# Performance work log

Measured on AMD Instinct MI355X. Metric: run time of the kernel, lower is better.

Reference implementation:

```python
import jax, jax.numpy as jnp
import numpy as np

B, P, E = 16, 1024, 768
HID, HEADS = 768, 12
DH = HID // HEADS  # 64
EPS = 1e-5


def setup_inputs() -> dict:
    key = jax.random.key(0)
    ks = jax.random.split(key, 4)
    return {
        "x": jax.random.normal(ks[0], (B, P, E), dtype=jnp.float32),
        "ln_weight": jnp.ones((P, E), dtype=jnp.float32),
        "ln_bias": jnp.zeros((P, E), dtype=jnp.float32),
        "qkv": jax.random.normal(ks[1], (E, 3 * HID), dtype=jnp.float32),
        "lin_w": jax.random.normal(ks[2], (HID, E), dtype=jnp.float32) * 0.02,
        "lin_b": jax.random.normal(ks[3], (E,), dtype=jnp.float32) * 0.02,
    }


def reference(x, ln_weight, ln_bias, qkv, lin_w, lin_b):
    # LayerNorm over the last TWO dims (patches, emb), per torch nn.LayerNorm((P, E))
    mean = jnp.mean(x, axis=(-2, -1), keepdims=True)
    var = jnp.var(x, axis=(-2, -1), keepdims=True)
    xn = (x - mean) / jnp.sqrt(var + EPS) * ln_weight + ln_bias

    # QKV projection: [B,P,E] @ [E,3*HID] -> [B,P,3*HID]
    proj = xn @ qkv
    # view(B,P,heads,-1) then permute -> [B,heads,P,3*DH]; chunk along last dim
    proj = proj.reshape(B, P, HEADS, 3 * DH).transpose(0, 2, 1, 3)
    q, k, v = proj[..., :DH], proj[..., DH:2 * DH], proj[..., 2 * DH:]

    # Softmax-free attention: (Q K^T) V
    atten = jnp.einsum("bhqd,bhkd->bhqk", q, k)  # [B,H,P,P]
    out = jnp.einsum("bhqk,bhkd->bhqd", atten, v)  # [B,H,P,DH]

    out = out.transpose(0, 2, 1, 3).reshape(B, P, HID)
    # dropout p=0.0 (eval) -> identity
    out = jax.nn.relu(out @ lin_w + lin_b)
    return out + x
```

## Files before the change

kernel.cpp:

```cpp
#include <hip/hip_runtime.h>
#include <hip/hip_bf16.h>
#include <cstdint>

#define BB   16
#define PP   1024
#define EE   768
#define HID  768
#define NH   12
#define DH   64
#define NPB  (PP * EE)
#define MROWS (BB * PP)

typedef __bf16 bf16_t;
typedef __bf16 bf16x8 __attribute__((ext_vector_type(8)));
typedef float  f32x4  __attribute__((ext_vector_type(4)));

__device__ __forceinline__ void gld16(const void* g, void* l) {
    __builtin_amdgcn_global_load_lds(
        (const __attribute__((address_space(1))) void*)(uintptr_t)g,
        (__attribute__((address_space(3))) void*)(uint32_t)(uintptr_t)l,
        16, 0, 0);
}

__global__ __launch_bounds__(256) void stats1_kernel(const float* __restrict__ x,
                                                     float* __restrict__ part) {
    int bid = blockIdx.x;
    int b = bid >> 6, s = bid & 63;
    const float4* xp = (const float4*)(x + (size_t)b * NPB + (size_t)s * 12288);
    float sum = 0.f, ss = 0.f;
#pragma unroll
    for (int i = 0; i < 12; ++i) {
        float4 v = xp[i * 256 + threadIdx.x];
        sum += v.x + v.y + v.z + v.w;
        ss  += v.x * v.x + v.y * v.y + v.z * v.z + v.w * v.w;
    }
#pragma unroll
    for (int off = 32; off > 0; off >>= 1) {
        sum += __shfl_down(sum, off, 64);
        ss  += __shfl_down(ss,  off, 64);
    }
    __shared__ float tmp[8];
    int wave = threadIdx.x >> 6, lane = threadIdx.x & 63;
    if (lane == 0) { tmp[wave * 2] = sum; tmp[wave * 2 + 1] = ss; }
    __syncthreads();
    if (threadIdx.x == 0) {
        part[bid * 2]     = tmp[0] + tmp[2] + tmp[4] + tmp[6];
        part[bid * 2 + 1] = tmp[1] + tmp[3] + tmp[5] + tmp[7];
    }
}

__global__ __launch_bounds__(256) void prep_kernel(const float* __restrict__ qkvw,
                                                   const float* __restrict__ linw,
                                                   const float* __restrict__ part,
                                                   bf16_t* __restrict__ qkvT,
                                                   bf16_t* __restrict__ lwT,
                                                   float* __restrict__ stats) {
    int bid = blockIdx.x;
    if (bid < 6912) {
        int idx = bid * 256 + threadIdx.x;
        int c = idx / 768, r = idx - c * 768;
        qkvT[idx] = (bf16_t)qkvw[(size_t)r * 2304 + c];
    } else if (bid < 9216) {
        int idx = (bid - 6912) * 256 + threadIdx.x;
        int c = idx / 768, r = idx - c * 768;
        lwT[idx] = (bf16_t)linw[(size_t)r * 768 + c];
    } else {
        int wave = threadIdx.x >> 6, lane = threadIdx.x & 63;
#pragma unroll
        for (int j = 0; j < 4; ++j) {
            int b = wave * 4 + j;
            float sum = part[(b * 64 + lane) * 2];
            float ss  = part[(b * 64 + lane) * 2 + 1];
#pragma unroll
            for (int off = 32; off > 0; off >>= 1) {
                sum += __shfl_down(sum, off, 64);
                ss  += __shfl_down(ss,  off, 64);
            }
            if (lane == 0) {
                const float inv_n = 1.f / (float)NPB;
                float mean = sum * inv_n;
                float var  = ss * inv_n - mean * mean;
                stats[b * 2]     = mean;
                stats[b * 2 + 1] = rsqrtf(var + 1e-5f);
            }
        }
    }
}

__global__ __launch_bounds__(256) void ln_apply_kernel(const float* __restrict__ x,
                                                       const float* __restrict__ lnw,
                                                       const float* __restrict__ lnb,
                                                       const float* __restrict__ stats,
                                                       bf16_t* __restrict__ xn) {
    int i = (blockIdx.x * 256 + threadIdx.x) * 8;
    int b = i / NPB;
    int r = i - b * NPB;
    float mean = stats[b * 2], rstd = stats[b * 2 + 1];
    float4 x0 = *(const float4*)(x + i),     x1 = *(const float4*)(x + i + 4);
    float4 w0 = *(const float4*)(lnw + r),   w1 = *(const float4*)(lnw + r + 4);
    float4 c0 = *(const float4*)(lnb + r),   c1 = *(const float4*)(lnb + r + 4);
    union { bf16_t h[8]; uint4 u; } o;
    o.h[0] = (bf16_t)((x0.x - mean) * rstd * w0.x + c0.x);
    o.h[1] = (bf16_t)((x0.y - mean) * rstd * w0.y + c0.y);
    o.h[2] = (bf16_t)((x0.z - mean) * rstd * w0.z + c0.z);
    o.h[3] = (bf16_t)((x0.w - mean) * rstd * w0.w + c0.w);
    o.h[4] = (bf16_t)((x1.x - mean) * rstd * w1.x + c1.x);
    o.h[5] = (bf16_t)((x1.y - mean) * rstd * w1.y + c1.y);
    o.h[6] = (bf16_t)((x1.z - mean) * rstd * w1.z + c1.z);
    o.h[7] = (bf16_t)((x1.w - mean) * rstd * w1.w + c1.w);
    *(uint4*)(xn + i) = o.u;
}

template <int KDIM>
__device__ __forceinline__ void gemm_core_128(const bf16_t* __restrict__ A,
                                              const bf16_t* __restrict__ Bt,
                                              int mBase, int nBase,
                                              f32x4 acc[4][4],
                                              bf16_t* As, bf16_t* Bs) {
    const int t = threadIdx.x;
    const int lane = t & 63, wave = t >> 6;
    const int wm = wave >> 1, wn = wave & 1;
    const int m16 = lane & 15, quad = lane >> 4;

    const int sr = t >> 3, s8 = t & 7;
    const bf16_t* pa[4]; const bf16_t* pb[4];
#pragma unroll
    for (int i = 0; i < 4; ++i) {
        int row = i * 32 + sr;
        int g = (s8 - (row & 7)) & 7;
        pa[i] = A  + (size_t)(mBase + row) * KDIM + g * 8;
        pb[i] = Bt + (size_t)(nBase + row) * KDIM + g * 8;
    }

    int raOff[4][2], rbOff[4][2];
#pragma unroll
    for (int i = 0; i < 4; ++i) {
        int ra = wm * 64 + i * 16 + m16;
        int rb = wn * 64 + i * 16 + m16;
#pragma unroll
        for (int ks = 0; ks < 2; ++ks) {
            raOff[i][ks] = ra * 64 + (((ks * 4 + quad) + (ra & 7)) & 7) * 8;
            rbOff[i][ks] = rb * 64 + (((ks * 4 + quad) + (rb & 7)) & 7) * 8;
        }
    }

    const f32x4 z = {0.f, 0.f, 0.f, 0.f};
#pragma unroll
    for (int mm = 0; mm < 4; ++mm)
#pragma unroll
        for (int nn = 0; nn < 4; ++nn) acc[mm][nn] = z;

    for (int k0 = 0; k0 < KDIM; k0 += 64) {
        __syncthreads();
#pragma unroll
        for (int i = 0; i < 4; ++i) {
            gld16(pa[i] + k0, As + i * 2048 + t * 8);
            gld16(pb[i] + k0, Bs + i * 2048 + t * 8);
        }
        __syncthreads();
#pragma unroll
        for (int ks = 0; ks < 2; ++ks) {
            bf16x8 af[4], bfv[4];
#pragma unroll
            for (int i = 0; i < 4; ++i) {
                af[i]  = *(const bf16x8*)(As + raOff[i][ks]);
                bfv[i] = *(const bf16x8*)(Bs + rbOff[i][ks]);
            }
#pragma unroll
            for (int mm = 0; mm < 4; ++mm)
#pragma unroll
                for (int nn = 0; nn < 4; ++nn)
                    acc[mm][nn] = __builtin_amdgcn_mfma_f32_16x16x32_bf16(
                        af[mm], bfv[nn], acc[mm][nn], 0, 0, 0);
        }
    }
}

__global__ __launch_bounds__(256) void gemm_qkv_kernel(const bf16_t* __restrict__ xn,
                                                       const bf16_t* __restrict__ qkvT,
                                                       bf16_t* __restrict__ q,
                                                       bf16_t* __restrict__ kt,
                                                       bf16_t* __restrict__ vt) {
    __shared__ bf16_t smem[16384];
    f32x4 acc[4][4];
    const int mBase = blockIdx.y * 128, nBase = blockIdx.x * 128;
    gemm_core_128<768>(xn, qkvT, mBase, nBase, acc, smem, smem + 8192);

    const int t = threadIdx.x;
    const int lane = t & 63, wave = t >> 6;
    const int wm = wave >> 1, wn = wave & 1;
    const int m16 = lane & 15, quad = lane >> 4;
    const int b = mBase >> 10, p0 = mBase & 1023;

#pragma unroll
    for (int half = 0; half < 2; ++half) {
        const int g = blockIdx.x * 2 + half;
        const int cls = g % 3, h = g / 3;
        const size_t bh = (size_t)(b * NH + h);
        __syncthreads();
        if (cls == 0) {
            if (wn == half) {
#pragma unroll
                for (int mm = 0; mm < 4; ++mm)
#pragma unroll
                    for (int nn = 0; nn < 4; ++nn)
#pragma unroll
                        for (int i = 0; i < 4; ++i)
                            smem[(wm * 64 + mm * 16 + quad * 4 + i) * 72 + nn * 16 + m16] =
                                (bf16_t)acc[mm][nn][i];
            }
            __syncthreads();
#pragma unroll
            for (int it = 0; it < 4; ++it) {
                int slot = it * 256 + t;
                int r = slot >> 3, cc = slot & 7;
                bf16x8 val = *(const bf16x8*)(smem + r * 72 + cc * 8);
                *(bf16x8*)(q + ((size_t)(b * PP + p0 + r)) * HID + h * DH + cc * 8) = val;
            }
        } else {
            bf16_t* dst = (cls == 1) ? kt : vt;
            if (wn == half) {
#pragma unroll
                for (int mm = 0; mm < 4; ++mm)
#pragma unroll
                    for (int nn = 0; nn < 4; ++nn) {
                        int c = nn * 16 + m16;
                        int r0 = wm * 64 + mm * 16 + quad * 4;
                        union { bf16_t hh[4]; uint2 u; } pk;
#pragma unroll
                        for (int i = 0; i < 4; ++i) pk.hh[i] = (bf16_t)acc[mm][nn][i];
                        *(uint2*)(&smem[c * 136 + r0]) = pk.u;
                    }
            }
            __syncthreads();
#pragma unroll
            for (int it = 0; it < 4; ++it) {
                int slot = it * 256 + t;
                int d = slot >> 4, pc = slot & 15;
                bf16x8 val = *(const bf16x8*)(smem + d * 136 + pc * 8);
                *(bf16x8*)(dst + (bh * DH + d) * PP + p0 + pc * 8) = val;
            }
        }
    }
}

__global__ __launch_bounds__(256) void kv_kernel(const bf16_t* __restrict__ kt,
                                                 const bf16_t* __restrict__ vt,
                                                 bf16_t* __restrict__ thi,
                                                 bf16_t* __restrict__ tlo) {
    __shared__ float red[4 * 64 * 65];
    const int bh = blockIdx.x;
    const bf16_t* Kb = kt + (size_t)bh * DH * PP;
    const bf16_t* Vb = vt + (size_t)bh * DH * PP;
    const int t = threadIdx.x;
    const int lane = t & 63, wave = t >> 6;
    const int m16 = lane & 15, quad = lane >> 4;
    const f32x4 z = {0.f, 0.f, 0.f, 0.f};
    f32x4 acc[4][4];
#pragma unroll
    for (int mm = 0; mm < 4; ++mm)
#pragma unroll
        for (int nn = 0; nn < 4; ++nn) acc[mm][nn] = z;

    for (int ks = 0; ks < 8; ++ks) {
        int kb = wave * 256 + ks * 32 + quad * 8;
        bf16x8 af[4], bfv[4];
#pragma unroll
        for (int mm = 0; mm < 4; ++mm)
            af[mm] = *(const bf16x8*)(Kb + (size_t)(mm * 16 + m16) * PP + kb);
#pragma unroll
        for (int nn = 0; nn < 4; ++nn)
            bfv[nn] = *(const bf16x8*)(Vb + (size_t)(nn * 16 + m16) * PP + kb);
#pragma unroll
        for (int mm = 0; mm < 4; ++mm)
#pragma unroll
            for (int nn = 0; nn < 4; ++nn)
                acc[mm][nn] = __builtin_amdgcn_mfma_f32_16x16x32_bf16(
                    af[mm], bfv[nn], acc[mm][nn], 0, 0, 0);
    }
#pragma unroll
    for (int mm = 0; mm < 4; ++mm)
#pragma unroll
        for (int nn = 0; nn < 4; ++nn)
#pragma unroll
            for (int i = 0; i < 4; ++i)
                red[wave * 4160 + (mm * 16 + quad * 4 + i) * 65 + nn * 16 + m16] =
                    acc[mm][nn][i];
    __syncthreads();
#pragma unroll
    for (int j = 0; j < 16; ++j) {
        int idx = j * 256 + t;
        int m = idx >> 6, n = idx & 63;
        int a = m * 65 + n;
        float s = red[a] + red[4160 + a] + red[8320 + a] + red[12480 + a];
        bf16_t hi = (bf16_t)s;
        float lo = s - (float)hi;
        thi[(size_t)bh * 4096 + idx] = hi;
        tlo[(size_t)bh * 4096 + idx] = (bf16_t)lo;
    }
}

__global__ __launch_bounds__(256) void u_kernel(const bf16_t* __restrict__ thi,
                                                const bf16_t* __restrict__ tlo,
                                                const bf16_t* __restrict__ lwT,
                                                bf16_t* __restrict__ ut) {
    const int bh = blockIdx.x;
    const int b = bh / NH, h = bh - b * NH;
    const int nBase = blockIdx.y * 256;
    const bf16_t* Th = thi + (size_t)bh * 4096;
    const bf16_t* Tl = tlo + (size_t)bh * 4096;
    const int t = threadIdx.x, lane = t & 63, wave = t >> 6;
    const int wm = wave >> 1, wn = wave & 1;
    const int m16 = lane & 15, quad = lane >> 4;
    const f32x4 z = {0.f, 0.f, 0.f, 0.f};
    f32x4 acc[2][8];
#pragma unroll
    for (int mm = 0; mm < 2; ++mm)
#pragma unroll
        for (int nn = 0; nn < 8; ++nn) acc[mm][nn] = z;

#pragma unroll
    for (int ks = 0; ks < 2; ++ks) {
        bf16x8 ah[2], al[2], bfr[8];
#pragma unroll
        for (int mm = 0; mm < 2; ++mm) {
            ah[mm] = *(const bf16x8*)(Th + (wm * 32 + mm * 16 + m16) * 64 + ks * 32 + quad * 8);
            al[mm] = *(const bf16x8*)(Tl + (wm * 32 + mm * 16 + m16) * 64 + ks * 32 + quad * 8);
        }
#pragma unroll
        for (int nn = 0; nn < 8; ++nn)
            bfr[nn] = *(const bf16x8*)(
                lwT + (size_t)(nBase + wn * 128 + nn * 16 + m16) * 768 + h * 64 + ks * 32 + quad * 8);
#pragma unroll
        for (int mm = 0; mm < 2; ++mm)
#pragma unroll
            for (int nn = 0; nn < 8; ++nn) {
                acc[mm][nn] = __builtin_amdgcn_mfma_f32_16x16x32_bf16(
                    ah[mm], bfr[nn], acc[mm][nn], 0, 0, 0);
                acc[mm][nn] = __builtin_amdgcn_mfma_f32_16x16x32_bf16(
                    al[mm], bfr[nn], acc[mm][nn], 0, 0, 0);
            }
    }
#pragma unroll
    for (int mm = 0; mm < 2; ++mm)
#pragma unroll
        for (int nn = 0; nn < 8; ++nn) {
            int e  = nBase + wn * 128 + nn * 16 + m16;
            int d1 = wm * 32 + mm * 16 + quad * 4;
            union { bf16_t hh[4]; uint2 u; } pk;
#pragma unroll
            for (int i = 0; i < 4; ++i) pk.hh[i] = (bf16_t)acc[mm][nn][i];
            *(uint2*)(ut + ((size_t)b * 768 + e) * 768 + h * 64 + d1) = pk.u;
        }
}

__global__ __launch_bounds__(256) void gemm_out_kernel(const bf16_t* __restrict__ q,
                                                       const bf16_t* __restrict__ ut,
                                                       const float* __restrict__ linb,
                                                       const float* __restrict__ x,
                                                       float* __restrict__ out) {
    __shared__ bf16_t smem[16384];
    f32x4 acc[4][4];
    const int mBase = blockIdx.y * 128, nBase = blockIdx.x * 128;
    const int b = mBase >> 10;
    gemm_core_128<768>(q, ut + (size_t)b * 768 * 768, mBase, nBase, acc,
                       smem, smem + 8192);

    const int lane = threadIdx.x & 63, wave = threadIdx.x >> 6;
    const int wm = wave >> 1, wn = wave & 1;
    const int m16 = lane & 15, quad = lane >> 4;
#pragma unroll
    for (int mm = 0; mm < 4; ++mm) {
#pragma unroll
        for (int i = 0; i < 4; ++i) {
            size_t row = mBase + wm * 64 + mm * 16 + quad * 4 + i;
#pragma unroll
            for (int nn = 0; nn < 4; ++nn) {
                int col = nBase + wn * 64 + nn * 16 + m16;
                float v = acc[mm][nn][i] + linb[col];
                v = fmaxf(v, 0.f) + x[row * EE + col];
                out[row * EE + col] = v;
            }
        }
    }
}

extern "C" void kernel_launch(void* const* d_in, const int* in_sizes, int n_in,
                              void* d_out, int out_size, void* d_ws, size_t ws_size,
                              hipStream_t stream) {
    const float* x    = (const float*)d_in[0];
    const float* lnw  = (const float*)d_in[1];
    const float* lnb  = (const float*)d_in[2];
    const float* qkvw = (const float*)d_in[3];
    const float* linw = (const float*)d_in[4];
    const float* linb = (const float*)d_in[5];
    float* out = (float*)d_out;
    char* ws = (char*)d_ws;

    float*  part  = (float*)(ws + 0);
    float*  stats = (float*)(ws + 8192);
    bf16_t* xn    = (bf16_t*)(ws + 8448);
    bf16_t* qkvT  = (bf16_t*)(ws + 25174272);
    bf16_t* lwT   = (bf16_t*)(ws + 28713216);
    bf16_t* q     = (bf16_t*)(ws + 29892864);
    bf16_t* kt    = (bf16_t*)(ws + 55058688);
    bf16_t* vt    = (bf16_t*)(ws + 80224512);
    bf16_t* thi   = qkvT;
    bf16_t* tlo   = qkvT + 192 * 4096;
    bf16_t* ut    = kt;

    stats1_kernel<<<dim3(BB * 64), dim3(256), 0, stream>>>(x, part);
    prep_kernel<<<dim3(9217), dim3(256), 0, stream>>>(qkvw, linw, part, qkvT, lwT, stats);
    ln_apply_kernel<<<dim3(6144), dim3(256), 0, stream>>>(x, lnw, lnb, stats, xn);
    gemm_qkv_kernel<<<dim3(18, 128), dim3(256), 0, stream>>>(xn, qkvT, q, kt, vt);
    kv_kernel<<<dim3(192), dim3(256), 0, stream>>>(kt, vt, thi, tlo);
    u_kernel<<<dim3(192, 3), dim3(256), 0, stream>>>(thi, tlo, lwT, ut);
    gemm_out_kernel<<<dim3(6, 128), dim3(256), 0, stream>>>(q, ut, linb, x, out);
}
```

Before: 288.6 us.

## Use 256x128 GEMM tiles with 512 threads and tile the weight transpose

The QKV and output GEMMs move from 128x128 tiles with 256 threads to 256x128 tiles with 512 threads (8 waves), so each B tile loaded into LDS is reused across twice as many rows. The epilogues are adjusted for the larger tile. The weight transpose/cast in prep_kernel now goes through a swizzled 64x64 shared-memory tile, so both global reads and writes are coalesced instead of strided. The bigger LDS footprint and fewer blocks may lower occupancy and leave the last wave of work unbalanced.

```diff
diff --git a/kernel.cpp b/kernel.cpp
--- a/kernel.cpp
+++ b/kernel.cpp
@@ -56,14 +56,33 @@
                                                    bf16_t* __restrict__ lwT,
                                                    float* __restrict__ stats) {
     int bid = blockIdx.x;
-    if (bid < 6912) {
-        int idx = bid * 256 + threadIdx.x;
-        int c = idx / 768, r = idx - c * 768;
-        qkvT[idx] = (bf16_t)qkvw[(size_t)r * 2304 + c];
-    } else if (bid < 9216) {
-        int idx = (bid - 6912) * 256 + threadIdx.x;
-        int c = idx / 768, r = idx - c * 768;
-        lwT[idx] = (bf16_t)linw[(size_t)r * 768 + c];
+    if (bid < 576) {
+        const float* src; bf16_t* dst; int R, C, tr, tc;
+        if (bid < 432) { src = qkvw; dst = qkvT; R = 768; C = 2304; tr = bid / 36; tc = bid % 36; }
+        else { int i2 = bid - 432; src = linw; dst = lwT; R = 768; C = 768; tr = i2 / 12; tc = i2 % 12; }
+        __shared__ bf16_t Ls[64 * 72];
+        const int r0 = tr * 64, c0 = tc * 64;
+        const int t = threadIdx.x;
+#pragma unroll
+        for (int it = 0; it < 4; ++it) {
+            int idx = it * 256 + t;
+            int r = idx >> 4, cq = idx & 15;
+            float4 v = *(const float4*)(src + (size_t)(r0 + r) * C + c0 + cq * 4);
+            float vv[4] = {v.x, v.y, v.z, v.w};
+#pragma unroll
+            for (int j = 0; j < 4; ++j) {
+                int c = cq * 4 + j;
+                Ls[c * 72 + (((r >> 3) ^ (c & 7)) << 3) + (r & 7)] = (bf16_t)vv[j];
+            }
+        }
+        __syncthreads();
+#pragma unroll
+        for (int it = 0; it < 2; ++it) {
+            int idx = it * 256 + t;
+            int c = idx >> 3, rq = idx & 7;
+            bf16x8 val = *(const bf16x8*)(Ls + c * 72 + ((rq ^ (c & 7)) << 3));
+            *(bf16x8*)(dst + (size_t)(c0 + c) * R + r0 + rq * 8) = val;
+        }
     } else {
         int wave = threadIdx.x >> 6, lane = threadIdx.x & 63;
 #pragma unroll
@@ -112,7 +131,7 @@
 }
 
 template <int KDIM>
-__device__ __forceinline__ void gemm_core_128(const bf16_t* __restrict__ A,
+__device__ __forceinline__ void gemm_core_256(const bf16_t* __restrict__ A,
                                               const bf16_t* __restrict__ Bt,
                                               int mBase, int nBase,
                                               f32x4 acc[4][4],
@@ -123,12 +142,17 @@
     const int m16 = lane & 15, quad = lane >> 4;
 
     const int sr = t >> 3, s8 = t & 7;
-    const bf16_t* pa[4]; const bf16_t* pb[4];
+    const bf16_t* pa[4]; const bf16_t* pb[2];
 #pragma unroll
     for (int i = 0; i < 4; ++i) {
-        int row = i * 32 + sr;
+        int row = i * 64 + sr;
         int g = (s8 - (row & 7)) & 7;
-        pa[i] = A  + (size_t)(mBase + row) * KDIM + g * 8;
+        pa[i] = A + (size_t)(mBase + row) * KDIM + g * 8;
+    }
+#pragma unroll
+    for (int i = 0; i < 2; ++i) {
+        int row = i * 64 + sr;
+        int g = (s8 - (row & 7)) & 7;
         pb[i] = Bt + (size_t)(nBase + row) * KDIM + g * 8;
     }
 
@@ -153,10 +177,9 @@
     for (int k0 = 0; k0 < KDIM; k0 += 64) {
         __syncthreads();
 #pragma unroll
-        for (int i = 0; i < 4; ++i) {
-            gld16(pa[i] + k0, As + i * 2048 + t * 8);
-            gld16(pb[i] + k0, Bs + i * 2048 + t * 8);
-        }
+        for (int i = 0; i < 4; ++i) gld16(pa[i] + k0, As + i * 4096 + t * 8);
+#pragma unroll
+        for (int i = 0; i < 2; ++i) gld16(pb[i] + k0, Bs + i * 4096 + t * 8);
         __syncthreads();
 #pragma unroll
         for (int ks = 0; ks < 2; ++ks) {
@@ -176,15 +199,15 @@
     }
 }
 
-__global__ __launch_bounds__(256) void gemm_qkv_kernel(const bf16_t* __restrict__ xn,
+__global__ __launch_bounds__(512) void gemm_qkv_kernel(const bf16_t* __restrict__ xn,
                                                        const bf16_t* __restrict__ qkvT,
                                                        bf16_t* __restrict__ q,
                                                        bf16_t* __restrict__ kt,
                                                        bf16_t* __restrict__ vt) {
-    __shared__ bf16_t smem[16384];
+    __shared__ bf16_t smem[24576];
     f32x4 acc[4][4];
-    const int mBase = blockIdx.y * 128, nBase = blockIdx.x * 128;
-    gemm_core_128<768>(xn, qkvT, mBase, nBase, acc, smem, smem + 8192);
+    const int mBase = blockIdx.y * 256, nBase = blockIdx.x * 128;
+    gemm_core_256<768>(xn, qkvT, mBase, nBase, acc, smem, smem + 16384);
 
     const int t = threadIdx.x;
     const int lane = t & 63, wave = t >> 6;
@@ -212,7 +235,7 @@
             __syncthreads();
 #pragma unroll
             for (int it = 0; it < 4; ++it) {
-                int slot = it * 256 + t;
+                int slot = it * 512 + t;
                 int r = slot >> 3, cc = slot & 7;
                 bf16x8 val = *(const bf16x8*)(smem + r * 72 + cc * 8);
                 *(bf16x8*)(q + ((size_t)(b * PP + p0 + r)) * HID + h * DH + cc * 8) = val;
@@ -229,15 +252,15 @@
                         union { bf16_t hh[4]; uint2 u; } pk;
 #pragma unroll
                         for (int i = 0; i < 4; ++i) pk.hh[i] = (bf16_t)acc[mm][nn][i];
-                        *(uint2*)(&smem[c * 136 + r0]) = pk.u;
+                        *(uint2*)(&smem[c * 264 + r0]) = pk.u;
                     }
             }
             __syncthreads();
 #pragma unroll
             for (int it = 0; it < 4; ++it) {
-                int slot = it * 256 + t;
-                int d = slot >> 4, pc = slot & 15;
-                bf16x8 val = *(const bf16x8*)(smem + d * 136 + pc * 8);
+                int slot = it * 512 + t;
+                int d = slot >> 5, pc = slot & 31;
+                bf16x8 val = *(const bf16x8*)(smem + d * 264 + pc * 8);
                 *(bf16x8*)(dst + (bh * DH + d) * PP + p0 + pc * 8) = val;
             }
         }
@@ -354,17 +377,17 @@
         }
 }
 
-__global__ __launch_bounds__(256) void gemm_out_kernel(const bf16_t* __restrict__ q,
+__global__ __launch_bounds__(512) void gemm_out_kernel(const bf16_t* __restrict__ q,
                                                        const bf16_t* __restrict__ ut,
                                                        const float* __restrict__ linb,
                                                        const float* __restrict__ x,
                                                        float* __restrict__ out) {
-    __shared__ bf16_t smem[16384];
+    __shared__ bf16_t smem[24576];
     f32x4 acc[4][4];
-    const int mBase = blockIdx.y * 128, nBase = blockIdx.x * 128;
+    const int mBase = blockIdx.y * 256, nBase = blockIdx.x * 128;
     const int b = mBase >> 10;
-    gemm_core_128<768>(q, ut + (size_t)b * 768 * 768, mBase, nBase, acc,
-                       smem, smem + 8192);
+    gemm_core_256<768>(q, ut + (size_t)b * 768 * 768, mBase, nBase, acc,
+                       smem, smem + 16384);
 
     const int lane = threadIdx.x & 63, wave = threadIdx.x >> 6;
     const int wm = wave >> 1, wn = wave & 1;
@@ -410,10 +433,10 @@
     bf16_t* ut    = kt;
 
     stats1_kernel<<<dim3(BB * 64), dim3(256), 0, stream>>>(x, part);
-    prep_kernel<<<dim3(9217), dim3(256), 0, stream>>>(qkvw, linw, part, qkvT, lwT, stats);
+    prep_kernel<<<dim3(577), dim3(256), 0, stream>>>(qkvw, linw, part, qkvT, lwT, stats);
     ln_apply_kernel<<<dim3(6144), dim3(256), 0, stream>>>(x, lnw, lnb, stats, xn);
-    gemm_qkv_kernel<<<dim3(18, 128), dim3(256), 0, stream>>>(xn, qkvT, q, kt, vt);
+    gemm_qkv_kernel<<<dim3(18, 64), dim3(512), 0, stream>>>(xn, qkvT, q, kt, vt);
     kv_kernel<<<dim3(192), dim3(256), 0, stream>>>(kt, vt, thi, tlo);
     u_kernel<<<dim3(192, 3), dim3(256), 0, stream>>>(thi, tlo, lwT, ut);
-    gemm_out_kernel<<<dim3(6, 128), dim3(256), 0, stream>>>(q, ut, linb, x, out);
-}
+    gemm_out_kernel<<<dim3(6, 64), dim3(512), 0, stream>>>(q, ut, linb, x, out);
+}
```

Measured after the change: 302.8 us. 4.9% more time.
